# Kernel tuning notes

Hardware: AMD Instinct MI355X
Metric: run time of the kernel (lower is better)

## Reference

```python
import jax, jax.numpy as jnp
import numpy as np

H = 5  # hidden size (hardcoded in the torch module)


def setup_inputs() -> dict:
    key = jax.random.key(0)
    ks = jax.random.split(key, 9)
    N, T = 32768, 600
    s = 1.0 / np.sqrt(H)  # torch LSTM/Linear init scale (uniform bound), use as stddev
    return {
        "x": jax.random.normal(ks[0], (N, T), dtype=jnp.float32),
        "w_ih": jax.random.normal(ks[1], (4 * H, 1), dtype=jnp.float32) * s,
        "w_hh": jax.random.normal(ks[2], (4 * H, H), dtype=jnp.float32) * s,
        "b_ih": jax.random.normal(ks[3], (4 * H,), dtype=jnp.float32) * s,
        "b_hh": jax.random.normal(ks[4], (4 * H,), dtype=jnp.float32) * s,
        "fc_w": jax.random.normal(ks[5], (15, H), dtype=jnp.float32) * s,
        "fc_b": jax.random.normal(ks[6], (15,), dtype=jnp.float32) * s,
        "out_w": jax.random.normal(ks[7], (1, 15), dtype=jnp.float32) * (1.0 / np.sqrt(15)),
        "out_b": jax.random.normal(ks[8], (1,), dtype=jnp.float32) * (1.0 / np.sqrt(15)),
    }


def reference(x, w_ih, w_hh, b_ih, b_hh, fc_w, fc_b, out_w, out_b):
    # x: (N, T) -> unsqueeze to feature dim of 1 is implicit (input_size=1).
    N = x.shape[0]
    b = b_ih + b_hh  # (4H,)
    w_ih_vec = w_ih[:, 0]  # (4H,) since input_size == 1

    def step(carry, x_t):
        h, c = carry  # (N, H) each
        # gates: (N, 4H); PyTorch gate order: i, f, g, o
        gates = x_t[:, None] * w_ih_vec + h @ w_hh.T + b
        i = jax.nn.sigmoid(gates[:, 0 * H:1 * H])
        f = jax.nn.sigmoid(gates[:, 1 * H:2 * H])
        g = jnp.tanh(gates[:, 2 * H:3 * H])
        o = jax.nn.sigmoid(gates[:, 3 * H:4 * H])
        c = f * c + i * g
        h = o * jnp.tanh(c)
        return (h, c), None

    h0 = jnp.zeros((N, H), dtype=x.dtype)
    c0 = jnp.zeros((N, H), dtype=x.dtype)
    (h_T, _), _ = jax.lax.scan(step, (h0, c0), x.T)  # scan over time: xs (T, N)
    # Head: only the last timestep's hidden state is used.
    hid = h_T @ fc_w.T + fc_b          # (N, 15)
    out = hid @ out_w.T + out_b        # (N, 1)
    return jax.nn.sigmoid(out)
```

## Files before the change

kernel.cpp:

```cpp
#include <hip/hip_runtime.h>
#include <math.h>


#define LOG2E 1.44269504088896340736f

typedef float v2f __attribute__((ext_vector_type(2)));

constexpr int T_ = 600;
constexpr int SEQ_PER_BLOCK = 32;
constexpr int TTILE = 64;
constexpr int LDS_STRIDE = 68;

__device__ __forceinline__ float fast_rcp(float v)  { return __builtin_amdgcn_rcpf(v); }
__device__ __forceinline__ float fast_exp2(float v) { return __builtin_amdgcn_exp2f(v); }

__device__ __forceinline__ float dpp_swap1(float v) {
    const int x = __float_as_int(v);
    return __int_as_float(__builtin_amdgcn_update_dpp(x, x, 0xB1, 0xF, 0xF, false));
}

__global__ __launch_bounds__(64, 1) void lstm_kernel(
    const float* __restrict__ x,
    const float* __restrict__ w_ih,
    const float* __restrict__ w_hh,
    const float* __restrict__ b_ih,
    const float* __restrict__ b_hh,
    const float* __restrict__ fc_w,
    const float* __restrict__ fc_b,
    const float* __restrict__ out_w,
    const float* __restrict__ out_b,
    float* __restrict__ out)
{
    __shared__ float xs[SEQ_PER_BLOCK * LDS_STRIDE];

    const int lane = threadIdx.x;
    const int s    = lane >> 1;
    const int half = lane & 1;
    const int seq  = blockIdx.x * SEQ_PER_BLOCK + s;

    const float slo = -LOG2E;
    const float shi = half ? -LOG2E : -2.0f * LOG2E;
    v2f wih2[5], bb2[5], whh2[5][5];
#pragma unroll
    for (int p = 0; p < 5; ++p) {
        const int rlo = half * 5 + p;
        const int rhi = 10 + half * 5 + p;
        wih2[p] = (v2f){ w_ih[rlo] * slo, w_ih[rhi] * shi };
        bb2[p]  = (v2f){ (b_ih[rlo] + b_hh[rlo]) * slo,
                         (b_ih[rhi] + b_hh[rhi]) * shi };
#pragma unroll
        for (int k = 0; k < 5; ++k)
            whh2[p][k] = (v2f){ w_hh[rlo * 5 + k] * slo, w_hh[rhi * 5 + k] * shi };
    }
    const float Ahi = half ? 1.0f : 2.0f;
    const float Bhi = half ? 0.0f : -1.0f;

    float h[5] = {0.f, 0.f, 0.f, 0.f, 0.f};
    float c[5] = {0.f, 0.f, 0.f, 0.f, 0.f};

    const float* xblk = x + (size_t)(blockIdx.x * SEQ_PER_BLOCK) * T_;

    auto step = [&](float xt) {
        const v2f x2 = (v2f){ xt, xt };
        v2f g2[5];
#pragma unroll
        for (int p = 0; p < 5; ++p) g2[p] = x2 * wih2[p] + bb2[p];
#pragma unroll
        for (int k = 0; k < 5; ++k) {
            const v2f h2 = (v2f){ h[k], h[k] };
#pragma unroll
            for (int p = 0; p < 5; ++p) g2[p] += h2 * whh2[p][k];
        }
        float actl[5], acth[5];
#pragma unroll
        for (int p = 0; p < 5; ++p) {
            actl[p] = fast_rcp(1.0f + fast_exp2(g2[p].x));
            acth[p] = fmaf(fast_rcp(1.0f + fast_exp2(g2[p].y)), Ahi, Bhi);
        }
        float sl[5], sh[5];
#pragma unroll
        for (int k = 0; k < 5; ++k) { sl[k] = dpp_swap1(actl[k]); sh[k] = dpp_swap1(acth[k]); }
#pragma unroll
        for (int k = 0; k < 5; ++k) {
            const float t0 = actl[k] * acth[k];
            const float t1 = sl[k] * sh[k];
            const float ig = half ? t1 : t0;
            const float fv = half ? actl[k] : sl[k];
            c[k] = fmaf(fv, c[k], ig);
            const float e  = fast_exp2(c[k] * (-2.0f * LOG2E));
            const float tc = fmaf(fast_rcp(1.0f + e), 2.0f, -1.0f);
            const float ov = half ? acth[k] : sh[k];
            h[k] = ov * tc;
        }
    };

    const int rrow = lane >> 4;
    const int ccol = (lane & 15) << 2;

    for (int t0 = 0; t0 < T_; t0 += TTILE) {
        __syncthreads();
#pragma unroll
        for (int it = 0; it < 8; ++it) {
            const int r = it * 4 + rrow;
            if (t0 + ccol < T_) {
                const float4 v = *(const float4*)(xblk + (size_t)r * T_ + (t0 + ccol));
                *(float4*)&xs[r * LDS_STRIDE + ccol] = v;
            }
        }
        __syncthreads();

        const int steps = min(TTILE, T_ - t0);
        const float* xr = &xs[s * LDS_STRIDE];
        for (int tt = 0; tt < steps; tt += 4) {
            const float4 xv4 = *(const float4*)&xr[tt];
            step(xv4.x);
            step(xv4.y);
            step(xv4.z);
            step(xv4.w);
        }
    }

    if (half == 0) {
        float acc = out_b[0];
#pragma unroll
        for (int j = 0; j < 15; ++j) {
            float hid = fc_b[j];
#pragma unroll
            for (int k = 0; k < 5; ++k) hid = fmaf(h[k], fc_w[j * 5 + k], hid);
            acc = fmaf(hid, out_w[j], acc);
        }
        out[seq] = fast_rcp(1.0f + fast_exp2(-acc * LOG2E));
    }
}

extern "C" void kernel_launch(void* const* d_in, const int* in_sizes, int n_in,
                              void* d_out, int out_size, void* d_ws, size_t ws_size,
                              hipStream_t stream) {
    const float* x    = (const float*)d_in[0];
    const float* w_ih = (const float*)d_in[1];
    const float* w_hh = (const float*)d_in[2];
    const float* b_ih = (const float*)d_in[3];
    const float* b_hh = (const float*)d_in[4];
    const float* fc_w = (const float*)d_in[5];
    const float* fc_b = (const float*)d_in[6];
    const float* out_w = (const float*)d_in[7];
    const float* out_b = (const float*)d_in[8];
    float* out = (float*)d_out;

    const int N = in_sizes[0] / T_;
    const int grid = N / SEQ_PER_BLOCK;
    hipLaunchKernelGGL(lstm_kernel, dim3(grid), dim3(64), 0, stream,
                       x, w_ih, w_hh, b_ih, b_hh, fc_w, fc_b, out_w, out_b, out);
}
```

Before: 301.6 us.

## Rebalance LSTM gate split across lane pair, share reciprocals, double-buffer x tiles

Reassigns hidden units across the two lanes of each sequence so each lane owns 2.5 cell states (two full plus one shared), cutting transcendental work per step, and merges pairs of reciprocals into one rcp via a product trick. It also double-buffers the x tile in LDS, prefetching the next tile into registers while computing the current one, to hide global load latency. This adds DPP quad permutes and risks precision loss from the shared reciprocal products and overflow when the exp terms are large.

```diff
diff --git a/kernel.cpp b/kernel.cpp
--- a/kernel.cpp
+++ b/kernel.cpp
@@ -9,14 +9,17 @@
 constexpr int T_ = 600;
 constexpr int SEQ_PER_BLOCK = 32;
 constexpr int TTILE = 64;
+constexpr int NTILES = (T_ + TTILE - 1) / TTILE;
 constexpr int LDS_STRIDE = 68;
+constexpr int XBUF = SEQ_PER_BLOCK * LDS_STRIDE;
 
 __device__ __forceinline__ float fast_rcp(float v)  { return __builtin_amdgcn_rcpf(v); }
 __device__ __forceinline__ float fast_exp2(float v) { return __builtin_amdgcn_exp2f(v); }
 
-__device__ __forceinline__ float dpp_swap1(float v) {
+template <int CTRL>
+__device__ __forceinline__ float dpp_q(float v) {
     const int x = __float_as_int(v);
-    return __int_as_float(__builtin_amdgcn_update_dpp(x, x, 0xB1, 0xF, 0xF, false));
+    return __int_as_float(__builtin_amdgcn_update_dpp(x, x, CTRL, 0xF, 0xF, false));
 }
 
 __global__ __launch_bounds__(64, 1) void lstm_kernel(
@@ -31,32 +34,36 @@
     const float* __restrict__ out_b,
     float* __restrict__ out)
 {
-    __shared__ float xs[SEQ_PER_BLOCK * LDS_STRIDE];
+    __shared__ float xs[2 * XBUF];
 
     const int lane = threadIdx.x;
     const int s    = lane >> 1;
     const int half = lane & 1;
     const int seq  = blockIdx.x * SEQ_PER_BLOCK + s;
 
-    const float slo = -LOG2E;
-    const float shi = half ? -LOG2E : -2.0f * LOG2E;
-    v2f wih2[5], bb2[5], whh2[5][5];
+    const int rloT[2][5] = {{0, 1, 2, 5, 6}, {3, 4, 7, 8, 9}};
+    const int rhiT[2][5] = {{10, 11, 12, 15, 16}, {13, 14, 17, 18, 19}};
+    const int gtT [2][5] = {{1, 1, 1, 0, 0}, {1, 1, 0, 0, 0}};
+
+    v2f wih2[5], bb2[5], whh2[5][5], A2[5], B2[5];
 #pragma unroll
     for (int p = 0; p < 5; ++p) {
-        const int rlo = half * 5 + p;
-        const int rhi = 10 + half * 5 + p;
-        wih2[p] = (v2f){ w_ih[rlo] * slo, w_ih[rhi] * shi };
-        bb2[p]  = (v2f){ (b_ih[rlo] + b_hh[rlo]) * slo,
-                         (b_ih[rhi] + b_hh[rhi]) * shi };
+        const int rlo = rloT[half][p], rhi = rhiT[half][p];
+        const int gt  = gtT[half][p];
+        const float sl = -LOG2E;
+        const float sh = gt ? (-2.0f * LOG2E) : (-LOG2E);
+        wih2[p] = (v2f){ w_ih[rlo] * sl, w_ih[rhi] * sh };
+        bb2[p]  = (v2f){ (b_ih[rlo] + b_hh[rlo]) * sl,
+                         (b_ih[rhi] + b_hh[rhi]) * sh };
 #pragma unroll
         for (int k = 0; k < 5; ++k)
-            whh2[p][k] = (v2f){ w_hh[rlo * 5 + k] * slo, w_hh[rhi * 5 + k] * shi };
+            whh2[p][k] = (v2f){ w_hh[rlo * 5 + k] * sl, w_hh[rhi * 5 + k] * sh };
+        A2[p] = (v2f){ 1.0f, gt ? (-4.0f * LOG2E) : 1.0f };
+        B2[p] = (v2f){ 0.0f, gt ? ( 2.0f * LOG2E) : 0.0f };
     }
-    const float Ahi = half ? 1.0f : 2.0f;
-    const float Bhi = half ? 0.0f : -1.0f;
 
-    float h[5] = {0.f, 0.f, 0.f, 0.f, 0.f};
-    float c[5] = {0.f, 0.f, 0.f, 0.f, 0.f};
+    float H[5] = {0.f, 0.f, 0.f, 0.f, 0.f};
+    float cA = 0.f, cB = 0.f, cC = 0.f;
 
     const float* xblk = x + (size_t)(blockIdx.x * SEQ_PER_BLOCK) * T_;
 
@@ -67,56 +74,86 @@
         for (int p = 0; p < 5; ++p) g2[p] = x2 * wih2[p] + bb2[p];
 #pragma unroll
         for (int k = 0; k < 5; ++k) {
-            const v2f h2 = (v2f){ h[k], h[k] };
+            const v2f h2 = (v2f){ H[k], H[k] };
 #pragma unroll
             for (int p = 0; p < 5; ++p) g2[p] += h2 * whh2[p][k];
         }
-        float actl[5], acth[5];
+        v2f act2[5];
 #pragma unroll
         for (int p = 0; p < 5; ++p) {
-            actl[p] = fast_rcp(1.0f + fast_exp2(g2[p].x));
-            acth[p] = fmaf(fast_rcp(1.0f + fast_exp2(g2[p].y)), Ahi, Bhi);
+            v2f d2;
+            d2.x = 1.0f + fast_exp2(g2[p].x);
+            d2.y = 1.0f + fast_exp2(g2[p].y);
+            const float rp = fast_rcp(d2.x * d2.y);
+            const v2f r2 = (v2f){ rp * d2.y, rp * d2.x };
+            act2[p] = r2 * A2[p] + B2[p];
         }
-        float sl[5], sh[5];
-#pragma unroll
-        for (int k = 0; k < 5; ++k) { sl[k] = dpp_swap1(actl[k]); sh[k] = dpp_swap1(acth[k]); }
-#pragma unroll
-        for (int k = 0; k < 5; ++k) {
-            const float t0 = actl[k] * acth[k];
-            const float t1 = sl[k] * sh[k];
-            const float ig = half ? t1 : t0;
-            const float fv = half ? actl[k] : sl[k];
-            c[k] = fmaf(fv, c[k], ig);
-            const float e  = fast_exp2(c[k] * (-2.0f * LOG2E));
-            const float tc = fmaf(fast_rcp(1.0f + e), 2.0f, -1.0f);
-            const float ov = half ? acth[k] : sh[k];
-            h[k] = ov * tc;
-        }
+        const float PA = act2[0].x * act2[0].y;
+        const float PB = act2[1].x * act2[1].y;
+        const float P2 = dpp_q<0xA0>(act2[2].x * act2[2].y);
+        const float f2 = dpp_q<0xF5>(act2[2].x);
+        const float o2 = dpp_q<0xF5>(act2[2].y);
+        cA = fmaf(act2[3].x, cA, PA);
+        cB = fmaf(act2[4].x, cB, PB);
+        cC = fmaf(f2, cC, P2);
+        const float dA = 1.0f + fast_exp2(cA);
+        const float dB = 1.0f + fast_exp2(cB);
+        const float dC = 1.0f + fast_exp2(cC);
+        const float q  = fast_rcp(dA * dB);
+        const float tA = fmaf(q * dB, 2.0f, -1.0f);
+        const float tB = fmaf(q * dA, 2.0f, -1.0f);
+        const float tC = fmaf(fast_rcp(dC), 2.0f, -1.0f);
+        const float hA = act2[3].y * tA;
+        const float hB = act2[4].y * tB;
+        const float hC = o2 * tC;
+        H[0] = dpp_q<0xA0>(hA);
+        H[1] = dpp_q<0xA0>(hB);
+        H[2] = hC;
+        H[3] = dpp_q<0xF5>(hA);
+        H[4] = dpp_q<0xF5>(hB);
     };
 
     const int rrow = lane >> 4;
     const int ccol = (lane & 15) << 2;
 
-    for (int t0 = 0; t0 < T_; t0 += TTILE) {
-        __syncthreads();
 #pragma unroll
-        for (int it = 0; it < 8; ++it) {
-            const int r = it * 4 + rrow;
-            if (t0 + ccol < T_) {
-                const float4 v = *(const float4*)(xblk + (size_t)r * T_ + (t0 + ccol));
-                *(float4*)&xs[r * LDS_STRIDE + ccol] = v;
+    for (int it = 0; it < 8; ++it) {
+        const int r = it * 4 + rrow;
+        const float4 v = *(const float4*)(xblk + (size_t)r * T_ + ccol);
+        *(float4*)&xs[r * LDS_STRIDE + ccol] = v;
+    }
+    __syncthreads();
+
+    for (int tile = 0; tile < NTILES; ++tile) {
+        float4 pf[8];
+        const int tn  = tile + 1;
+        const int t0n = tn * TTILE;
+        if (tn < NTILES) {
+#pragma unroll
+            for (int it = 0; it < 8; ++it) {
+                const int r = it * 4 + rrow;
+                if (t0n + ccol < T_)
+                    pf[it] = *(const float4*)(xblk + (size_t)r * T_ + (t0n + ccol));
             }
         }
-        __syncthreads();
-
-        const int steps = min(TTILE, T_ - t0);
-        const float* xr = &xs[s * LDS_STRIDE];
+        const int t0i  = tile * TTILE;
+        const int steps = min(TTILE, T_ - t0i);
+        const float* xr = &xs[(tile & 1) * XBUF + s * LDS_STRIDE];
         for (int tt = 0; tt < steps; tt += 4) {
             const float4 xv4 = *(const float4*)&xr[tt];
             step(xv4.x);
             step(xv4.y);
             step(xv4.z);
             step(xv4.w);
+        }
+        if (tn < NTILES) {
+#pragma unroll
+            for (int it = 0; it < 8; ++it) {
+                const int r = it * 4 + rrow;
+                if (t0n + ccol < T_)
+                    *(float4*)&xs[(tn & 1) * XBUF + r * LDS_STRIDE + ccol] = pf[it];
+            }
+            __syncthreads();
         }
     }
 
@@ -126,7 +163,7 @@
         for (int j = 0; j < 15; ++j) {
             float hid = fc_b[j];
 #pragma unroll
-            for (int k = 0; k < 5; ++k) hid = fmaf(h[k], fc_w[j * 5 + k], hid);
+            for (int k = 0; k < 5; ++k) hid = fmaf(H[k], fc_w[j * 5 + k], hid);
             acc = fmaf(hid, out_w[j], acc);
         }
         out[seq] = fast_rcp(1.0f + fast_exp2(-acc * LOG2E));
```

Measured after the change: 260.8 us. 13.5% less time.
